# Optimization experiments

Measured on AMD Instinct MI355X. Metric: run time of the kernel, lower is better.

Reference implementation:

```python
import jax, jax.numpy as jnp
import numpy as np

N_NODES = 500000


def _gconv(x, src, dst, ew, w_neigh, b, w_self):
    # DGL GraphConv(norm='none'): multiply weight first (in>=out here), then aggregate.
    h = x @ w_neigh                      # [N, out]
    msg = h[src] * ew[:, None]           # [E, out]
    agg = jax.ops.segment_sum(msg, dst, num_segments=N_NODES)
    return agg + b + x @ w_self          # neigh conv (+bias) + self-loop linear (no bias)


def setup_inputs() -> dict:
    key = jax.random.key(0)
    ks = jax.random.split(key, 16)
    N, E, G, F = N_NODES, 16000000, 64, 16
    inp = {
        "x": jax.random.normal(ks[0], (N, F), jnp.float32),
        "src": jax.random.randint(ks[1], (E,), 0, N),
        "dst": jax.random.randint(ks[2], (E,), 0, N),
        "graph_id": jnp.sort(jax.random.randint(ks[3], (N,), 0, G)),
        "edge_weight": jax.random.uniform(ks[4], (E,), jnp.float32),
        "num_graphs": G,
        "w_neigh0": jax.random.normal(ks[5], (F, 1), jnp.float32),
        "b0": jax.random.normal(ks[6], (1,), jnp.float32),
        "w_self0": jax.random.normal(ks[7], (F, 1), jnp.float32),
        "w_neigh1": jax.random.normal(ks[8], (1, 1), jnp.float32),
        "b1": jax.random.normal(ks[9], (1,), jnp.float32),
        "w_self1": jax.random.normal(ks[10], (1, 1), jnp.float32),
        "w_neigh2": jax.random.normal(ks[11], (1, 1), jnp.float32),
        "b2": jax.random.normal(ks[12], (1,), jnp.float32),
        "w_self2": jax.random.normal(ks[13], (1, 1), jnp.float32),
        "fc1_w": jax.random.normal(ks[14], (8, 1), jnp.float32),
        "fc1_b": jax.random.normal(ks[15], (8,), jnp.float32),
        "out_w": jax.random.normal(jax.random.fold_in(key, 100), (4, 8), jnp.float32),
        "out_b": jax.random.normal(jax.random.fold_in(key, 101), (4,), jnp.float32),
    }
    return inp


def reference(x, src, dst, graph_id, edge_weight, num_graphs,
              w_neigh0, b0, w_self0, w_neigh1, b1, w_self1,
              w_neigh2, b2, w_self2, fc1_w, fc1_b, out_w, out_b):
    h = jax.nn.relu(_gconv(x, src, dst, edge_weight, w_neigh0, b0, w_self0))
    h = jax.nn.relu(_gconv(h, src, dst, edge_weight, w_neigh1, b1, w_self1))
    h = jax.nn.relu(_gconv(h, src, dst, edge_weight, w_neigh2, b2, w_self2))
    # dgl.sum_nodes: per-graph segment sum over batched graph -> [G, 1]
    hg = jax.ops.segment_sum(h, graph_id, num_segments=num_graphs)
    hg2 = jax.nn.sigmoid((hg @ fc1_w.T + fc1_b) * 1000.0)   # [G, 8]
    out = jax.nn.relu(hg2 @ out_w.T + out_b)                # [G, 4]
    return jax.nn.log_softmax(out, axis=1)
```

## Files before the change

kernel.cpp:

```cpp
#include <hip/hip_runtime.h>

#define N_NODES   500000
#define NGRAPH    64
#define FDIM      16
#define NPB       4096
#define NPB_SHIFT 12
#define NBINS     123
#define NBLK      1024
#define CH        4096
typedef unsigned int u32;
typedef unsigned long long u64;

__global__ __launch_bounds__(1024) void proj_hist(const int* __restrict__ dst, int E, int chunk,
                                                  u32* __restrict__ blockHist,
                                                  const float* __restrict__ x,
                                                  const float* __restrict__ wn,
                                                  const float* __restrict__ wsf,
                                                  float* __restrict__ a,
                                                  float* __restrict__ s) {
    __shared__ u32 cnt[NBINS];
    if (blockIdx.x < NBLK) {
        for (int t = threadIdx.x; t < NBINS; t += 1024) cnt[t] = 0;
        __syncthreads();
        int b = blockIdx.x;
        int lo = b * chunk, hi = min(lo + chunk, E);
        int m = (hi - lo) & ~3;
        for (int i = lo + threadIdx.x * 4; i < lo + m; i += 4096) {
            int4 d = *(const int4*)(dst + i);
            atomicAdd(&cnt[((u32)d.x) >> NPB_SHIFT], 1u);
            atomicAdd(&cnt[((u32)d.y) >> NPB_SHIFT], 1u);
            atomicAdd(&cnt[((u32)d.z) >> NPB_SHIFT], 1u);
            atomicAdd(&cnt[((u32)d.w) >> NPB_SHIFT], 1u);
        }
        for (int i = lo + m + threadIdx.x; i < hi; i += 1024)
            atomicAdd(&cnt[((u32)dst[i]) >> NPB_SHIFT], 1u);
        __syncthreads();
        for (int t = threadIdx.x; t < NBINS; t += 1024)
            blockHist[(size_t)b * NBINS + t] = cnt[t];
    } else {
        int i = (blockIdx.x - NBLK) * 1024 + threadIdx.x;
        if (i >= N_NODES) return;
        const float4* xr = (const float4*)(x + (size_t)i * FDIM);
        float4 v0 = xr[0], v1 = xr[1], v2 = xr[2], v3 = xr[3];
        const float4* n4 = (const float4*)wn;
        const float4* s4 = (const float4*)wsf;
        float4 n0 = n4[0], n1 = n4[1], n2 = n4[2], n3 = n4[3];
        float4 w0 = s4[0], w1 = s4[1], w2 = s4[2], w3 = s4[3];
        float an = v0.x*n0.x + v0.y*n0.y + v0.z*n0.z + v0.w*n0.w
                 + v1.x*n1.x + v1.y*n1.y + v1.z*n1.z + v1.w*n1.w
                 + v2.x*n2.x + v2.y*n2.y + v2.z*n2.z + v2.w*n2.w
                 + v3.x*n3.x + v3.y*n3.y + v3.z*n3.z + v3.w*n3.w;
        float as = v0.x*w0.x + v0.y*w0.y + v0.z*w0.z + v0.w*w0.w
                 + v1.x*w1.x + v1.y*w1.y + v1.z*w1.z + v1.w*w1.w
                 + v2.x*w2.x + v2.y*w2.y + v2.z*w2.z + v2.w*w2.w
                 + v3.x*w3.x + v3.y*w3.y + v3.z*w3.z + v3.w*w3.w;
        a[i] = an;
        s[i] = as;
    }
}

__global__ __launch_bounds__(NBLK) void scan1_kernel(u32* __restrict__ blockHist,
                                                     u32* __restrict__ binTotal) {
    int j = blockIdx.x;
    __shared__ u32 lsum[NBLK];
    int t = threadIdx.x;
    u32 v = blockHist[(size_t)t * NBINS + j];
    lsum[t] = v;
    __syncthreads();
    u32 x = v;
    for (int off = 1; off < NBLK; off <<= 1) {
        u32 y = (t >= off) ? lsum[t - off] : 0u;
        __syncthreads();
        x += y; lsum[t] = x;
        __syncthreads();
    }
    if (t == NBLK - 1) binTotal[j] = x;
    blockHist[(size_t)t * NBINS + j] = x - v;
}

__global__ void scan2_kernel(const u32* __restrict__ binTotal, u32* __restrict__ binStart) {
    __shared__ u32 sh[128];
    int t = threadIdx.x;
    u32 v = (t < NBINS) ? binTotal[t] : 0u;
    sh[t] = v;
    __syncthreads();
    for (int d = 1; d < 128; d <<= 1) {
        u32 y = (t >= d) ? sh[t - d] : 0u;
        __syncthreads();
        sh[t] += y;
        __syncthreads();
    }
    if (t < NBINS) binStart[t] = sh[t] - v;
    if (t == 127) binStart[NBINS] = sh[127];
}

__global__ __launch_bounds__(512) void scatter_staged(const int* __restrict__ src,
                                                      const int* __restrict__ dst,
                                                      const float* __restrict__ ew,
                                                      int E, int chunk,
                                                      const u32* __restrict__ blockHist,
                                                      const u32* __restrict__ binStart,
                                                      u64* __restrict__ binned) {
    __shared__ u32 cursor[NBINS];
    __shared__ u32 cnt[NBINS];
    __shared__ u32 off[NBINS];
    __shared__ u64 stage[CH];
    __shared__ unsigned char binOf[CH];
    int b   = blockIdx.x;
    int tid = threadIdx.x;
    for (int t = tid; t < NBINS; t += 512)
        cursor[t] = binStart[t] + blockHist[(size_t)b * NBINS + t];
    int lo = b * chunk, hiB = min(lo + chunk, E);
    for (int base = lo; base < hiB; base += CH) {
        int n = min(CH, hiB - base);
        for (int t = tid; t < NBINS; t += 512) cnt[t] = 0;
        __syncthreads();
        u32 rec[8]; float wv[8]; u32 bi[8]; u32 rk[8];
#pragma unroll
        for (int k = 0; k < 8; ++k) {
            int idx = base + k * 512 + tid;
            bi[k] = 0xFFFFFFFFu;
            if (idx < base + n) {
                u32 d  = (u32)dst[idx];
                bi[k]  = d >> NPB_SHIFT;
                rec[k] = ((u32)src[idx]) | ((d & (NPB - 1)) << 19);
                wv[k]  = ew[idx];
                rk[k]  = atomicAdd(&cnt[bi[k]], 1u);
            }
        }
        __syncthreads();
        if (tid < NBINS) off[tid] = cnt[tid];
        __syncthreads();
        for (int d2 = 1; d2 < 128; d2 <<= 1) {
            u32 v = 0;
            if (tid < NBINS) { v = off[tid]; if (tid >= d2) v += off[tid - d2]; }
            __syncthreads();
            if (tid < NBINS) off[tid] = v;
            __syncthreads();
        }
        if (tid < NBINS) off[tid] -= cnt[tid];
        __syncthreads();
#pragma unroll
        for (int k = 0; k < 8; ++k) {
            if (bi[k] != 0xFFFFFFFFu) {
                u32 p = off[bi[k]] + rk[k];
                stage[p] = (u64)rec[k] | ((u64)__float_as_uint(wv[k]) << 32);
                binOf[p] = (unsigned char)bi[k];
            }
        }
        __syncthreads();
        for (int p = tid; p < n; p += 512) {
            u32 j = binOf[p];
            binned[cursor[j] + ((u32)p - off[j])] = stage[p];
        }
        __syncthreads();
        for (int t = tid; t < NBINS; t += 512) cursor[t] += cnt[t];
        __syncthreads();
    }
}

template<int S>
__global__ __launch_bounds__(512) void bin_pass(const u64* __restrict__ binned,
                                                const u32* __restrict__ binStart,
                                                const float* __restrict__ hsrc,
                                                float* __restrict__ partials) {
    __shared__ float acc[NPB];
    int blk   = blockIdx.x;
    int j     = blk / S;
    int slice = blk % S;
    for (int t = threadIdx.x; t < NPB; t += 512) acc[t] = 0.0f;
    __syncthreads();
    u32 blo = binStart[j], bhi = binStart[j + 1];
    u32 cnt = bhi - blo;
    u32 per = (cnt + S - 1) / S;
    u32 lo = blo + slice * per;
    u32 hi = min(lo + per, bhi);

    u32 i = lo + threadIdx.x;
    for (; i + 7u * 512u < hi; i += 8u * 512u) {
        u64 e[8];
#pragma unroll
        for (int k = 0; k < 8; ++k) e[k] = __builtin_nontemporal_load(&binned[i + (u32)k * 512u]);
        float g[8];
#pragma unroll
        for (int k = 0; k < 8; ++k) g[k] = hsrc[((u32)e[k]) & 0x7FFFFu];
#pragma unroll
        for (int k = 0; k < 8; ++k)
            atomicAdd(&acc[((u32)e[k]) >> 19], g[k] * __uint_as_float((u32)(e[k] >> 32)));
    }
    for (; i < hi; i += 512) {
        u64 e = __builtin_nontemporal_load(&binned[i]);
        u32 xx = (u32)e;
        atomicAdd(&acc[xx >> 19], hsrc[xx & 0x7FFFFu] * __uint_as_float((u32)(e >> 32)));
    }
    __syncthreads();
    float* p = partials + (size_t)(j * S + slice) * NPB;
    for (int t = threadIdx.x; t < NPB; t += 512)
        __builtin_nontemporal_store(acc[t], &p[t]);
}

template<int S>
__global__ void merge_update(const float* __restrict__ partials,
                             const float* __restrict__ selfv,
                             const float* __restrict__ wnp,
                             const float* __restrict__ bp,
                             const float* __restrict__ wsp,
                             float* __restrict__ hout) {
    int n = blockIdx.x * blockDim.x + threadIdx.x;
    if (n >= N_NODES) return;
    int j = n >> NPB_SHIFT;
    int l = n & (NPB - 1);
    const float* p = partials + (size_t)j * S * NPB + l;
    float sum = 0.0f;
#pragma unroll
    for (int k = 0; k < S; ++k) sum += __builtin_nontemporal_load(&p[k * NPB]);
    float scale = wnp ? wnp[0] : 1.0f;
    float wself = wsp ? wsp[0] : 1.0f;
    hout[n] = fmaxf(sum * scale + bp[0] + selfv[n] * wself, 0.0f);
}

__global__ void edge_pass(const int* __restrict__ src, const int* __restrict__ dst,
                          const float* __restrict__ ew, const float* __restrict__ h,
                          float* __restrict__ agg, const float* __restrict__ wnp, int E) {
    float scale = wnp ? wnp[0] : 1.0f;
    int stride = gridDim.x * blockDim.x;
    for (int i = blockIdx.x * blockDim.x + threadIdx.x; i < E; i += stride)
        atomicAdd(&agg[dst[i]], h[src[i]] * ew[i] * scale);
}
__global__ void node_update(const float* __restrict__ agg, const float* __restrict__ selfv,
                            const float* __restrict__ bp, const float* __restrict__ wsp,
                            float* __restrict__ hout) {
    int i = blockIdx.x * blockDim.x + threadIdx.x;
    if (i >= N_NODES) return;
    float wsc = wsp ? wsp[0] : 1.0f;
    hout[i] = fmaxf(agg[i] + bp[0] + selfv[i] * wsc, 0.0f);
}
__global__ void proj_kernel(const float* __restrict__ x, const float* __restrict__ wn,
                            const float* __restrict__ wsf, float* __restrict__ a,
                            float* __restrict__ s) {
    int i = blockIdx.x * blockDim.x + threadIdx.x;
    if (i >= N_NODES) return;
    float an = 0.f, as = 0.f;
    for (int k = 0; k < FDIM; ++k) {
        float v = x[(size_t)i * FDIM + k];
        an += v * wn[k]; as += v * wsf[k];
    }
    a[i] = an; s[i] = as;
}

__global__ __launch_bounds__(256) void graph_sum(const float* __restrict__ h,
                                                 const int* __restrict__ gid,
                                                 float* __restrict__ hg) {
    __shared__ float loc[NGRAPH];
    int t = threadIdx.x;
    if (t < NGRAPH) loc[t] = 0.0f;
    __syncthreads();
    int nq = N_NODES / 4;
    int stride = gridDim.x * blockDim.x;
    for (int q = blockIdx.x * blockDim.x + t; q < nq; q += stride) {
        int4   g4 = *(const int4*)(gid + 4 * q);
        float4 h4 = *(const float4*)(h + 4 * q);
        int g0 = __shfl(g4.x, 0);
        bool uni = (g4.x == g0) & (g4.w == g0);
        if (__all(uni)) {
            float v = h4.x + h4.y + h4.z + h4.w;
#pragma unroll
            for (int o = 32; o > 0; o >>= 1) v += __shfl_down(v, o);
            if ((t & 63) == 0) atomicAdd(&loc[g0], v);
        } else {
            atomicAdd(&loc[g4.x], h4.x);
            atomicAdd(&loc[g4.y], h4.y);
            atomicAdd(&loc[g4.z], h4.z);
            atomicAdd(&loc[g4.w], h4.w);
        }
    }
    __syncthreads();
    if (t < NGRAPH) atomicAdd(&hg[t], loc[t]);
}

__global__ void head_kernel(const float* __restrict__ hg,
                            const float* __restrict__ fc1w, const float* __restrict__ fc1b,
                            const float* __restrict__ outw, const float* __restrict__ outb,
                            float* __restrict__ out) {
    int g = threadIdx.x;
    if (g >= NGRAPH) return;
    float v = hg[g];
    float t[8];
#pragma unroll
    for (int j = 0; j < 8; ++j) {
        float z = (v * fc1w[j] + fc1b[j]) * 1000.0f;
        t[j] = 1.0f / (1.0f + expf(-z));
    }
    float o[4];
#pragma unroll
    for (int k = 0; k < 4; ++k) {
        float acc2 = outb[k];
#pragma unroll
        for (int j = 0; j < 8; ++j) acc2 += t[j] * outw[k * 8 + j];
        o[k] = fmaxf(acc2, 0.0f);
    }
    float m = fmaxf(fmaxf(o[0], o[1]), fmaxf(o[2], o[3]));
    float se = 0.0f;
#pragma unroll
    for (int k = 0; k < 4; ++k) se += expf(o[k] - m);
    float lse = m + logf(se);
#pragma unroll
    for (int k = 0; k < 4; ++k) out[g * 4 + k] = o[k] - lse;
}

extern "C" void kernel_launch(void* const* d_in, const int* in_sizes, int n_in,
                              void* d_out, int out_size, void* d_ws, size_t ws_size,
                              hipStream_t stream) {
    const float* x    = (const float*)d_in[0];
    const int*   src  = (const int*)  d_in[1];
    const int*   dst  = (const int*)  d_in[2];
    const int*   gid  = (const int*)  d_in[3];
    const float* ew   = (const float*)d_in[4];
    const float* wn0  = (const float*)d_in[6];
    const float* b0   = (const float*)d_in[7];
    const float* ws0  = (const float*)d_in[8];
    const float* wn1  = (const float*)d_in[9];
    const float* b1   = (const float*)d_in[10];
    const float* ws1  = (const float*)d_in[11];
    const float* wn2  = (const float*)d_in[12];
    const float* b2   = (const float*)d_in[13];
    const float* ws2  = (const float*)d_in[14];
    const float* fc1w = (const float*)d_in[15];
    const float* fc1b = (const float*)d_in[16];
    const float* outw = (const float*)d_in[17];
    const float* outb = (const float*)d_in[18];
    int E = in_sizes[1];

    const int BLK = 256;
    int nodeGrid = (N_NODES + BLK - 1) / BLK;
    char* ws = (char*)d_ws;

    size_t off = 0;
    u64*   binned    = (u64*)(ws + off);   off += (size_t)E * 8;
    u32*   blockHist = (u32*)(ws + off);   off += (size_t)NBLK * NBINS * 4;
    u32*   binStart  = (u32*)(ws + off);   off += (NBINS + 1) * 4;
    off = (off + 63) & ~(size_t)63;
    u32*   binTotal  = (u32*)(ws + off);   off += (NBINS + 1) * 4;
    off = (off + 63) & ~(size_t)63;
    float* partials  = (float*)(ws + off);
    size_t base_off  = off;
    size_t nodes_bytes = 4 * (size_t)N_NODES * 4 + NGRAPH * 4;
    size_t need8 = base_off + (size_t)NBINS * 8 * NPB * 4 + nodes_bytes;
    size_t need4 = base_off + (size_t)NBINS * 4 * NPB * 4 + nodes_bytes;

    int S = (ws_size >= need8) ? 8 : ((ws_size >= need4) ? 4 : 0);

    if (S) {
        off = base_off + (size_t)NBINS * S * NPB * 4;
        float* a  = (float*)(ws + off); off += (size_t)N_NODES * 4;
        float* s  = (float*)(ws + off); off += (size_t)N_NODES * 4;
        float* h0 = (float*)(ws + off); off += (size_t)N_NODES * 4;
        float* h1 = (float*)(ws + off); off += (size_t)N_NODES * 4;
        float* hg = (float*)(ws + off);

        int chunk = (((E + NBLK - 1) / NBLK) + 3) & ~3;
        int projBlocks = (N_NODES + 1023) / 1024;

        proj_hist<<<NBLK + projBlocks, 1024, 0, stream>>>(dst, E, chunk, blockHist,
                                                          x, wn0, ws0, a, s);
        scan1_kernel<<<NBINS, NBLK, 0, stream>>>(blockHist, binTotal);
        scan2_kernel<<<1, 128, 0, stream>>>(binTotal, binStart);
        scatter_staged<<<NBLK, 512, 0, stream>>>(src, dst, ew, E, chunk, blockHist, binStart, binned);

        if (S == 8) {
            bin_pass<8><<<NBINS * 8, 512, 0, stream>>>(binned, binStart, a, partials);
            merge_update<8><<<nodeGrid, BLK, 0, stream>>>(partials, s, nullptr, b0, nullptr, h0);
            bin_pass<8><<<NBINS * 8, 512, 0, stream>>>(binned, binStart, h0, partials);
            merge_update<8><<<nodeGrid, BLK, 0, stream>>>(partials, h0, wn1, b1, ws1, h1);
            bin_pass<8><<<NBINS * 8, 512, 0, stream>>>(binned, binStart, h1, partials);
            merge_update<8><<<nodeGrid, BLK, 0, stream>>>(partials, h1, wn2, b2, ws2, a);
        } else {
            bin_pass<4><<<NBINS * 4, 512, 0, stream>>>(binned, binStart, a, partials);
            merge_update<4><<<nodeGrid, BLK, 0, stream>>>(partials, s, nullptr, b0, nullptr, h0);
            bin_pass<4><<<NBINS * 4, 512, 0, stream>>>(binned, binStart, h0, partials);
            merge_update<4><<<nodeGrid, BLK, 0, stream>>>(partials, h0, wn1, b1, ws1, h1);
            bin_pass<4><<<NBINS * 4, 512, 0, stream>>>(binned, binStart, h1, partials);
            merge_update<4><<<nodeGrid, BLK, 0, stream>>>(partials, h1, wn2, b2, ws2, a);
        }

        (void)hipMemsetAsync(hg, 0, NGRAPH * sizeof(float), stream);
        graph_sum<<<512, 256, 0, stream>>>(a, gid, hg);
        head_kernel<<<1, 64, 0, stream>>>(hg, fc1w, fc1b, outw, outb, (float*)d_out);
    } else {
        float* wsb  = (float*)d_ws;
        float* fa   = wsb;
        float* fs   = wsb + 1 * (size_t)N_NODES;
        float* fagg = wsb + 2 * (size_t)N_NODES;
        float* fh   = wsb + 3 * (size_t)N_NODES;
        float* fhg  = wsb + 4 * (size_t)N_NODES;

        proj_kernel<<<nodeGrid, BLK, 0, stream>>>(x, wn0, ws0, fa, fs);

        (void)hipMemsetAsync(fagg, 0, (size_t)N_NODES * sizeof(float), stream);
        edge_pass<<<4096, BLK, 0, stream>>>(src, dst, ew, fa, fagg, nullptr, E);
        node_update<<<nodeGrid, BLK, 0, stream>>>(fagg, fs, b0, nullptr, fh);

        (void)hipMemsetAsync(fagg, 0, (size_t)N_NODES * sizeof(float), stream);
        edge_pass<<<4096, BLK, 0, stream>>>(src, dst, ew, fh, fagg, wn1, E);
        node_update<<<nodeGrid, BLK, 0, stream>>>(fagg, fh, b1, ws1, fh);

        (void)hipMemsetAsync(fagg, 0, (size_t)N_NODES * sizeof(float), stream);
        edge_pass<<<4096, BLK, 0, stream>>>(src, dst, ew, fh, fagg, wn2, E);
        node_update<<<nodeGrid, BLK, 0, stream>>>(fagg, fh, b2, ws2, fh);

        (void)hipMemsetAsync(fhg, 0, NGRAPH * sizeof(float), stream);
        graph_sum<<<512, 256, 0, stream>>>(fh, gid, fhg);
        head_kernel<<<1, 64, 0, stream>>>(fhg, fc1w, fc1b, outw, outb, (float*)d_out);
    }
}
```

Measured before the change: 408.6 us.

## Shrink binned edge records with fp16 weights, larger bins, fused graph sum

Splits the binned edge records into a 32-bit packed index array and a separate fp16 edge-weight array, cutting per-edge bytes read in each of the three aggregation passes from 8 to 6. Bins are widened to 8192 nodes (62 bins) with 16 slices per bin, and the per-graph sum is folded into the last merge_update through a wave-level reduction, which drops the graph_sum kernel. Node buffers are reused in place so only one workspace size path remains. Rounding edge weights to fp16 adds error relative to the fp32 reference, and the 32 KB shared accumulator per block may reduce occupancy.

```diff
diff --git a/kernel.cpp b/kernel.cpp
--- a/kernel.cpp
+++ b/kernel.cpp
@@ -1,14 +1,17 @@
 #include <hip/hip_runtime.h>
-
-#define N_NODES   500000
-#define NGRAPH    64
-#define FDIM      16
-#define NPB       4096
-#define NPB_SHIFT 12
-#define NBINS     123
-#define NBLK      1024
-#define CH        4096
+#include <hip/hip_fp16.h>
+
+#define N_NODES 500000
+#define NGRAPH  64
+#define FDIM    16
+#define NB1     62
+#define NPB1    8192
+#define SH1     13
+#define SLC     16
+#define NBLK    1024
+#define CH      4096
 typedef unsigned int u32;
+typedef unsigned short u16;
 typedef unsigned long long u64;
 
 __global__ __launch_bounds__(1024) void proj_hist(const int* __restrict__ dst, int E, int chunk,
@@ -18,25 +21,25 @@
                                                   const float* __restrict__ wsf,
                                                   float* __restrict__ a,
                                                   float* __restrict__ s) {
-    __shared__ u32 cnt[NBINS];
+    __shared__ u32 cnt[NB1];
     if (blockIdx.x < NBLK) {
-        for (int t = threadIdx.x; t < NBINS; t += 1024) cnt[t] = 0;
+        if (threadIdx.x < NB1) cnt[threadIdx.x] = 0;
         __syncthreads();
         int b = blockIdx.x;
         int lo = b * chunk, hi = min(lo + chunk, E);
         int m = (hi - lo) & ~3;
         for (int i = lo + threadIdx.x * 4; i < lo + m; i += 4096) {
             int4 d = *(const int4*)(dst + i);
-            atomicAdd(&cnt[((u32)d.x) >> NPB_SHIFT], 1u);
-            atomicAdd(&cnt[((u32)d.y) >> NPB_SHIFT], 1u);
-            atomicAdd(&cnt[((u32)d.z) >> NPB_SHIFT], 1u);
-            atomicAdd(&cnt[((u32)d.w) >> NPB_SHIFT], 1u);
+            atomicAdd(&cnt[((u32)d.x) >> SH1], 1u);
+            atomicAdd(&cnt[((u32)d.y) >> SH1], 1u);
+            atomicAdd(&cnt[((u32)d.z) >> SH1], 1u);
+            atomicAdd(&cnt[((u32)d.w) >> SH1], 1u);
         }
         for (int i = lo + m + threadIdx.x; i < hi; i += 1024)
-            atomicAdd(&cnt[((u32)dst[i]) >> NPB_SHIFT], 1u);
-        __syncthreads();
-        for (int t = threadIdx.x; t < NBINS; t += 1024)
-            blockHist[(size_t)b * NBINS + t] = cnt[t];
+            atomicAdd(&cnt[((u32)dst[i]) >> SH1], 1u);
+        __syncthreads();
+        if (threadIdx.x < NB1)
+            blockHist[(size_t)b * NB1 + threadIdx.x] = cnt[threadIdx.x];
     } else {
         int i = (blockIdx.x - NBLK) * 1024 + threadIdx.x;
         if (i >= N_NODES) return;
@@ -64,7 +67,7 @@
     int j = blockIdx.x;
     __shared__ u32 lsum[NBLK];
     int t = threadIdx.x;
-    u32 v = blockHist[(size_t)t * NBINS + j];
+    u32 v = blockHist[(size_t)t * NB1 + j];
     lsum[t] = v;
     __syncthreads();
     u32 x = v;
@@ -75,23 +78,23 @@
         __syncthreads();
     }
     if (t == NBLK - 1) binTotal[j] = x;
-    blockHist[(size_t)t * NBINS + j] = x - v;
+    blockHist[(size_t)t * NB1 + j] = x - v;
 }
 
 __global__ void scan2_kernel(const u32* __restrict__ binTotal, u32* __restrict__ binStart) {
-    __shared__ u32 sh[128];
+    __shared__ u32 sh[64];
     int t = threadIdx.x;
-    u32 v = (t < NBINS) ? binTotal[t] : 0u;
+    u32 v = (t < NB1) ? binTotal[t] : 0u;
     sh[t] = v;
     __syncthreads();
-    for (int d = 1; d < 128; d <<= 1) {
+    for (int d = 1; d < 64; d <<= 1) {
         u32 y = (t >= d) ? sh[t - d] : 0u;
         __syncthreads();
         sh[t] += y;
         __syncthreads();
     }
-    if (t < NBINS) binStart[t] = sh[t] - v;
-    if (t == 127) binStart[NBINS] = sh[127];
+    if (t < NB1) binStart[t] = sh[t] - v;
+    if (t == 63) binStart[NB1] = sh[63];
 }
 
 __global__ __launch_bounds__(512) void scatter_staged(const int* __restrict__ src,
@@ -100,123 +103,140 @@
                                                       int E, int chunk,
                                                       const u32* __restrict__ blockHist,
                                                       const u32* __restrict__ binStart,
-                                                      u64* __restrict__ binned) {
-    __shared__ u32 cursor[NBINS];
-    __shared__ u32 cnt[NBINS];
-    __shared__ u32 off[NBINS];
+                                                      u32* __restrict__ bIdx,
+                                                      u16* __restrict__ bW) {
+    __shared__ u32 cursor[64];
+    __shared__ u32 cnt[64];
+    __shared__ u32 off[64];
     __shared__ u64 stage[CH];
     __shared__ unsigned char binOf[CH];
-    int b   = blockIdx.x;
-    int tid = threadIdx.x;
-    for (int t = tid; t < NBINS; t += 512)
-        cursor[t] = binStart[t] + blockHist[(size_t)b * NBINS + t];
+    int b = blockIdx.x, tid = threadIdx.x;
+    if (tid < NB1) cursor[tid] = binStart[tid] + blockHist[(size_t)b * NB1 + tid];
     int lo = b * chunk, hiB = min(lo + chunk, E);
     for (int base = lo; base < hiB; base += CH) {
         int n = min(CH, hiB - base);
-        for (int t = tid; t < NBINS; t += 512) cnt[t] = 0;
-        __syncthreads();
-        u32 rec[8]; float wv[8]; u32 bi[8]; u32 rk[8];
+        if (tid < 64) cnt[tid] = 0;
+        __syncthreads();
+        u32 rec[8]; u16 wv[8]; u32 bi[8], rk[8];
 #pragma unroll
         for (int k = 0; k < 8; ++k) {
             int idx = base + k * 512 + tid;
             bi[k] = 0xFFFFFFFFu;
             if (idx < base + n) {
                 u32 d  = (u32)dst[idx];
-                bi[k]  = d >> NPB_SHIFT;
-                rec[k] = ((u32)src[idx]) | ((d & (NPB - 1)) << 19);
-                wv[k]  = ew[idx];
+                bi[k]  = d >> SH1;
+                rec[k] = ((u32)src[idx]) | ((d & (NPB1 - 1)) << 19);
+                wv[k]  = __half_as_ushort(__float2half(ew[idx]));
                 rk[k]  = atomicAdd(&cnt[bi[k]], 1u);
             }
         }
         __syncthreads();
-        if (tid < NBINS) off[tid] = cnt[tid];
-        __syncthreads();
-        for (int d2 = 1; d2 < 128; d2 <<= 1) {
-            u32 v = 0;
-            if (tid < NBINS) { v = off[tid]; if (tid >= d2) v += off[tid - d2]; }
+        if (tid < 64) off[tid] = cnt[tid];
+        __syncthreads();
+        for (int d2 = 1; d2 < 64; d2 <<= 1) {
+            u32 y = 0;
+            if (tid < 64 && tid >= d2) y = off[tid - d2];
             __syncthreads();
-            if (tid < NBINS) off[tid] = v;
+            if (tid < 64) off[tid] += y;
             __syncthreads();
         }
-        if (tid < NBINS) off[tid] -= cnt[tid];
+        if (tid < 64) off[tid] -= cnt[tid];
         __syncthreads();
 #pragma unroll
         for (int k = 0; k < 8; ++k) {
             if (bi[k] != 0xFFFFFFFFu) {
                 u32 p = off[bi[k]] + rk[k];
-                stage[p] = (u64)rec[k] | ((u64)__float_as_uint(wv[k]) << 32);
+                stage[p] = (u64)rec[k] | ((u64)wv[k] << 32);
                 binOf[p] = (unsigned char)bi[k];
             }
         }
         __syncthreads();
         for (int p = tid; p < n; p += 512) {
-            u32 j = binOf[p];
-            binned[cursor[j] + ((u32)p - off[j])] = stage[p];
-        }
-        __syncthreads();
-        for (int t = tid; t < NBINS; t += 512) cursor[t] += cnt[t];
-        __syncthreads();
-    }
-}
-
-template<int S>
-__global__ __launch_bounds__(512) void bin_pass(const u64* __restrict__ binned,
+            u32 jj = binOf[p];
+            u64 e = stage[p];
+            u32 gpos = cursor[jj] + ((u32)p - off[jj]);
+            bIdx[gpos] = (u32)e;
+            bW[gpos]   = (u16)(e >> 32);
+        }
+        __syncthreads();
+        if (tid < NB1) cursor[tid] += cnt[tid];
+        __syncthreads();
+    }
+}
+
+__global__ __launch_bounds__(512) void bin_pass(const u32* __restrict__ bIdx,
+                                                const u16* __restrict__ bW,
                                                 const u32* __restrict__ binStart,
                                                 const float* __restrict__ hsrc,
                                                 float* __restrict__ partials) {
-    __shared__ float acc[NPB];
-    int blk   = blockIdx.x;
-    int j     = blk / S;
-    int slice = blk % S;
-    for (int t = threadIdx.x; t < NPB; t += 512) acc[t] = 0.0f;
+    __shared__ float acc[NPB1];
+    int j = blockIdx.x / SLC, sl = blockIdx.x % SLC;
+    for (int t = threadIdx.x; t < NPB1; t += 512) acc[t] = 0.0f;
     __syncthreads();
     u32 blo = binStart[j], bhi = binStart[j + 1];
-    u32 cnt = bhi - blo;
-    u32 per = (cnt + S - 1) / S;
-    u32 lo = blo + slice * per;
+    u32 cj = bhi - blo;
+    u32 per = (cj + SLC - 1) / SLC;
+    u32 lo = blo + sl * per;
     u32 hi = min(lo + per, bhi);
-
     u32 i = lo + threadIdx.x;
     for (; i + 7u * 512u < hi; i += 8u * 512u) {
-        u64 e[8];
-#pragma unroll
-        for (int k = 0; k < 8; ++k) e[k] = __builtin_nontemporal_load(&binned[i + (u32)k * 512u]);
+        u32 r[8]; u16 w[8];
+#pragma unroll
+        for (int k = 0; k < 8; ++k) r[k] = __builtin_nontemporal_load(&bIdx[i + (u32)k * 512u]);
+#pragma unroll
+        for (int k = 0; k < 8; ++k) w[k] = __builtin_nontemporal_load(&bW[i + (u32)k * 512u]);
         float g[8];
 #pragma unroll
-        for (int k = 0; k < 8; ++k) g[k] = hsrc[((u32)e[k]) & 0x7FFFFu];
+        for (int k = 0; k < 8; ++k) g[k] = hsrc[r[k] & 0x7FFFFu];
 #pragma unroll
         for (int k = 0; k < 8; ++k)
-            atomicAdd(&acc[((u32)e[k]) >> 19], g[k] * __uint_as_float((u32)(e[k] >> 32)));
+            atomicAdd(&acc[r[k] >> 19], g[k] * __half2float(__ushort_as_half(w[k])));
     }
     for (; i < hi; i += 512) {
-        u64 e = __builtin_nontemporal_load(&binned[i]);
-        u32 xx = (u32)e;
-        atomicAdd(&acc[xx >> 19], hsrc[xx & 0x7FFFFu] * __uint_as_float((u32)(e >> 32)));
-    }
-    __syncthreads();
-    float* p = partials + (size_t)(j * S + slice) * NPB;
-    for (int t = threadIdx.x; t < NPB; t += 512)
+        u32 r = __builtin_nontemporal_load(&bIdx[i]);
+        u16 w = __builtin_nontemporal_load(&bW[i]);
+        atomicAdd(&acc[r >> 19], hsrc[r & 0x7FFFFu] * __half2float(__ushort_as_half(w)));
+    }
+    __syncthreads();
+    float* p = partials + ((size_t)j * SLC + sl) * NPB1;
+    for (int t = threadIdx.x; t < NPB1; t += 512)
         __builtin_nontemporal_store(acc[t], &p[t]);
 }
 
-template<int S>
-__global__ void merge_update(const float* __restrict__ partials,
-                             const float* __restrict__ selfv,
-                             const float* __restrict__ wnp,
-                             const float* __restrict__ bp,
-                             const float* __restrict__ wsp,
-                             float* __restrict__ hout) {
+template<bool LAST>
+__global__ __launch_bounds__(256) void merge_update(const float* __restrict__ partials,
+                                                    const float* __restrict__ selfv,
+                                                    const float* __restrict__ wnp,
+                                                    const float* __restrict__ bp,
+                                                    const float* __restrict__ wsp,
+                                                    float* __restrict__ hout,
+                                                    const int* __restrict__ gid,
+                                                    float* __restrict__ hg) {
     int n = blockIdx.x * blockDim.x + threadIdx.x;
     if (n >= N_NODES) return;
-    int j = n >> NPB_SHIFT;
-    int l = n & (NPB - 1);
-    const float* p = partials + (size_t)j * S * NPB + l;
+    int j = n >> SH1;
+    int l = n & (NPB1 - 1);
+    const float* p = partials + ((size_t)j * SLC) * NPB1 + l;
     float sum = 0.0f;
 #pragma unroll
-    for (int k = 0; k < S; ++k) sum += __builtin_nontemporal_load(&p[k * NPB]);
+    for (int k = 0; k < SLC; ++k) sum += __builtin_nontemporal_load(&p[k * NPB1]);
     float scale = wnp ? wnp[0] : 1.0f;
     float wself = wsp ? wsp[0] : 1.0f;
-    hout[n] = fmaxf(sum * scale + bp[0] + selfv[n] * wself, 0.0f);
+    float v = fmaxf(sum * scale + bp[0] + selfv[n] * wself, 0.0f);
+    hout[n] = v;
+    if (LAST) {
+        int g = gid[n];
+        unsigned long long act = __ballot(1);
+        int g0 = __shfl(g, 0);
+        if (act == ~0ull && __all(g == g0)) {
+            float t = v;
+#pragma unroll
+            for (int o = 32; o > 0; o >>= 1) t += __shfl_down(t, o);
+            if ((threadIdx.x & 63) == 0) atomicAdd(&hg[g0], t);
+        } else {
+            atomicAdd(&hg[g], v);
+        }
+    }
 }
 
 __global__ void edge_pass(const int* __restrict__ src, const int* __restrict__ dst,
@@ -336,55 +356,42 @@
     char* ws = (char*)d_ws;
 
     size_t off = 0;
-    u64*   binned    = (u64*)(ws + off);   off += (size_t)E * 8;
-    u32*   blockHist = (u32*)(ws + off);   off += (size_t)NBLK * NBINS * 4;
-    u32*   binStart  = (u32*)(ws + off);   off += (NBINS + 1) * 4;
+    u32* bIdx       = (u32*)(ws + off); off += (size_t)E * 4;
+    u16* bW         = (u16*)(ws + off); off += (size_t)E * 2;
     off = (off + 63) & ~(size_t)63;
-    u32*   binTotal  = (u32*)(ws + off);   off += (NBINS + 1) * 4;
+    u32* blockHist  = (u32*)(ws + off); off += (size_t)NBLK * NB1 * 4;
+    u32* binStart   = (u32*)(ws + off); off += (NB1 + 2) * 4;
     off = (off + 63) & ~(size_t)63;
-    float* partials  = (float*)(ws + off);
-    size_t base_off  = off;
-    size_t nodes_bytes = 4 * (size_t)N_NODES * 4 + NGRAPH * 4;
-    size_t need8 = base_off + (size_t)NBINS * 8 * NPB * 4 + nodes_bytes;
-    size_t need4 = base_off + (size_t)NBINS * 4 * NPB * 4 + nodes_bytes;
-
-    int S = (ws_size >= need8) ? 8 : ((ws_size >= need4) ? 4 : 0);
-
-    if (S) {
-        off = base_off + (size_t)NBINS * S * NPB * 4;
-        float* a  = (float*)(ws + off); off += (size_t)N_NODES * 4;
-        float* s  = (float*)(ws + off); off += (size_t)N_NODES * 4;
-        float* h0 = (float*)(ws + off); off += (size_t)N_NODES * 4;
-        float* h1 = (float*)(ws + off); off += (size_t)N_NODES * 4;
-        float* hg = (float*)(ws + off);
-
+    u32* binTotal   = (u32*)(ws + off); off += (NB1 + 2) * 4;
+    off = (off + 63) & ~(size_t)63;
+    float* partials = (float*)(ws + off); off += (size_t)NB1 * SLC * NPB1 * 4;
+    float* a  = (float*)(ws + off); off += (size_t)N_NODES * 4;
+    float* s  = (float*)(ws + off); off += (size_t)N_NODES * 4;
+    float* hg = (float*)(ws + off); off += 256;
+    size_t need = off;
+
+    if (ws_size >= need) {
         int chunk = (((E + NBLK - 1) / NBLK) + 3) & ~3;
         int projBlocks = (N_NODES + 1023) / 1024;
 
         proj_hist<<<NBLK + projBlocks, 1024, 0, stream>>>(dst, E, chunk, blockHist,
                                                           x, wn0, ws0, a, s);
-        scan1_kernel<<<NBINS, NBLK, 0, stream>>>(blockHist, binTotal);
-        scan2_kernel<<<1, 128, 0, stream>>>(binTotal, binStart);
-        scatter_staged<<<NBLK, 512, 0, stream>>>(src, dst, ew, E, chunk, blockHist, binStart, binned);
-
-        if (S == 8) {
-            bin_pass<8><<<NBINS * 8, 512, 0, stream>>>(binned, binStart, a, partials);
-            merge_update<8><<<nodeGrid, BLK, 0, stream>>>(partials, s, nullptr, b0, nullptr, h0);
-            bin_pass<8><<<NBINS * 8, 512, 0, stream>>>(binned, binStart, h0, partials);
-            merge_update<8><<<nodeGrid, BLK, 0, stream>>>(partials, h0, wn1, b1, ws1, h1);
-            bin_pass<8><<<NBINS * 8, 512, 0, stream>>>(binned, binStart, h1, partials);
-            merge_update<8><<<nodeGrid, BLK, 0, stream>>>(partials, h1, wn2, b2, ws2, a);
-        } else {
-            bin_pass<4><<<NBINS * 4, 512, 0, stream>>>(binned, binStart, a, partials);
-            merge_update<4><<<nodeGrid, BLK, 0, stream>>>(partials, s, nullptr, b0, nullptr, h0);
-            bin_pass<4><<<NBINS * 4, 512, 0, stream>>>(binned, binStart, h0, partials);
-            merge_update<4><<<nodeGrid, BLK, 0, stream>>>(partials, h0, wn1, b1, ws1, h1);
-            bin_pass<4><<<NBINS * 4, 512, 0, stream>>>(binned, binStart, h1, partials);
-            merge_update<4><<<nodeGrid, BLK, 0, stream>>>(partials, h1, wn2, b2, ws2, a);
-        }
-
+        scan1_kernel<<<NB1, NBLK, 0, stream>>>(blockHist, binTotal);
+        scan2_kernel<<<1, 64, 0, stream>>>(binTotal, binStart);
+        scatter_staged<<<NBLK, 512, 0, stream>>>(src, dst, ew, E, chunk, blockHist,
+                                                 binStart, bIdx, bW);
         (void)hipMemsetAsync(hg, 0, NGRAPH * sizeof(float), stream);
-        graph_sum<<<512, 256, 0, stream>>>(a, gid, hg);
+
+        bin_pass<<<NB1 * SLC, 512, 0, stream>>>(bIdx, bW, binStart, a, partials);
+        merge_update<false><<<nodeGrid, BLK, 0, stream>>>(partials, s, nullptr, b0, nullptr,
+                                                          s, gid, hg);
+        bin_pass<<<NB1 * SLC, 512, 0, stream>>>(bIdx, bW, binStart, s, partials);
+        merge_update<false><<<nodeGrid, BLK, 0, stream>>>(partials, s, wn1, b1, ws1,
+                                                          s, gid, hg);
+        bin_pass<<<NB1 * SLC, 512, 0, stream>>>(bIdx, bW, binStart, s, partials);
+        merge_update<true><<<nodeGrid, BLK, 0, stream>>>(partials, s, wn2, b2, ws2,
+                                                         s, gid, hg);
+
         head_kernel<<<1, 64, 0, stream>>>(hg, fc1w, fc1b, outw, outb, (float*)d_out);
     } else {
         float* wsb  = (float*)d_ws;
```

Measured after the change: 480.8 us. 17.7% more time.
